# Optimization experiments

Measured on AMD Instinct MI355X. Metric: run time of the kernel, lower is better.

Reference implementation:

```python
import jax, jax.numpy as jnp
import numpy as np

N_NODES = 20000
DIM = 128
N_EDGES = 500000
BATCH = 16384
EPS = 1e-6  # torch.nn.PairwiseDistance default eps


def setup_inputs() -> dict:
    key = jax.random.key(0)
    k = jax.random.split(key, 8)
    edges = jax.random.randint(k[0], (2, N_EDGES), 0, N_NODES, dtype=jnp.int64 if jax.config.jax_enable_x64 else jnp.int32)
    nodes_p_star = jnp.sort(jax.random.randint(k[1], (BATCH,), 0, N_NODES))
    nodes_p = jnp.sort(jax.random.randint(k[2], (BATCH,), 0, N_NODES))
    # learned parameters, init in [-1, 1) as in the torch module
    beta_p = 2.0 * jax.random.uniform(k[3], (N_NODES,), dtype=jnp.float32) - 1.0
    beta_p_star = 2.0 * jax.random.uniform(k[4], (N_NODES,), dtype=jnp.float32) - 1.0
    p = 2.0 * jax.random.uniform(k[5], (N_NODES, DIM), dtype=jnp.float32) - 1.0
    p_star = 2.0 * jax.random.uniform(k[6], (N_NODES, DIM), dtype=jnp.float32) - 1.0
    return {
        "edges": edges,
        "nodes_p_star": nodes_p_star,
        "nodes_p": nodes_p,
        "beta_p": beta_p,
        "beta_p_star": beta_p_star,
        "p": p,
        "p_star": p_star,
    }


def reference(edges, nodes_p_star, nodes_p, beta_p, beta_p_star, p, p_star):
    # ---- link term: sum over observed edges of (beta - dist) ----
    beta_pair = beta_p_star[edges[0]] + beta_p[edges[1]]  # [E]
    diff = p[edges[0]] - p_star[edges[1]]                 # [E, D]
    # torch PairwiseDistance adds eps to the difference before the norm
    z_dist = jnp.sqrt(jnp.sum((diff + EPS) ** 2, axis=-1))
    link_term = jnp.sum(beta_pair - z_dist)

    # ---- non-link term: triu-masked sum of exp(beta - cdist) ----
    bps = beta_p_star[nodes_p_star]   # [Ns]
    bp = beta_p[nodes_p]              # [Np]
    ps = p_star[nodes_p_star]         # [Ns, D]
    pp = p[nodes_p]                   # [Np, D]
    beta_mat = bps[None, :] + bp[:, None]          # [Np, Ns]
    # cdist(ps, pp) -> [Ns, Np] via Gram trick
    sq = (jnp.sum(ps * ps, axis=-1)[:, None]
          + jnp.sum(pp * pp, axis=-1)[None, :]
          - 2.0 * jnp.einsum('nd,md->nm', ps, pp))
    dist_mat = jnp.sqrt(jnp.maximum(sq, 0.0))      # [Ns, Np]
    intensity = jnp.exp(beta_mat.T - dist_mat)     # [Ns, Np]
    non_link = jnp.sum(jnp.triu(intensity, k=1))

    return -(link_term - non_link)
```

## Files before the change

### kernel.cpp

```cpp
#include <hip/hip_runtime.h>
#include <hip/hip_bf16.h>

#define N_NODES 20000
#define DIM 128
#define N_EDGES 500000
#define BATCH 16384
#define EPS 1e-6f
#define L2E 1.4426950408889634f

typedef _Float16 half8 __attribute__((ext_vector_type(8)));
typedef _Float16 half4_t __attribute__((ext_vector_type(4)));
typedef float f32x4 __attribute__((ext_vector_type(4)));

__device__ __forceinline__ float fast_sqrtf(float x) {
#if __has_builtin(__builtin_amdgcn_sqrtf)
    return __builtin_amdgcn_sqrtf(x);
#else
    return sqrtf(x);
#endif
}
__device__ __forceinline__ float fast_exp2f(float x) {
#if __has_builtin(__builtin_amdgcn_exp2f)
    return __builtin_amdgcn_exp2f(x);
#else
    return exp2f(x);
#endif
}

#define NB_TILE 8256

#define OFF_PGEMM 0
#define OFF_PSH   33280
#define OFF_PPH   4227584
#define OFF_N2S   8421888
#define OFF_N2P   8487424
#define OFF_BPS   8552960
#define OFF_BP    8618496
#define OFF_P16   8684032
#define OFF_PS16  13804032
#define OFF_END   18924032

__global__ __launch_bounds__(256) void prep_kernel(
    const float* __restrict__ p, const float* __restrict__ p_star,
    const float* __restrict__ beta_p, const float* __restrict__ beta_ps,
    const int* __restrict__ nodes_ps, const int* __restrict__ nodes_p,
    _Float16* __restrict__ Ah, float* __restrict__ n2A, float* __restrict__ bA2,
    _Float16* __restrict__ Bh, float* __restrict__ n2B, float* __restrict__ bB2,
    _Float16* __restrict__ p16, _Float16* __restrict__ ps16)
{
    const int bx = blockIdx.x;
    const int g = threadIdx.x & 31;
    const int r8 = threadIdx.x >> 5;
    if (bx < 4096) {
        const bool isA = bx < 2048;
        int row = (isA ? bx : bx - 2048) * 8 + r8;
        int id = isA ? nodes_ps[row] : nodes_p[row];
        const float* src = isA ? p_star : p;
        float4 v = ((const float4*)(src + (size_t)id * DIM))[g];
        half4_t o;
        o[0] = (_Float16)v.x; o[1] = (_Float16)v.y; o[2] = (_Float16)v.z; o[3] = (_Float16)v.w;
        _Float16* dst = isA ? Ah : Bh;
        *(half4_t*)(dst + (size_t)row * DIM + g * 4) = o;
        float nrm = v.x * v.x + v.y * v.y + v.z * v.z + v.w * v.w;
        #pragma unroll
        for (int m = 16; m >= 1; m >>= 1) nrm += __shfl_xor(nrm, m, 32);
        if (g == 0) {
            if (isA) { n2A[row] = nrm; bA2[row] = L2E * beta_ps[id]; }
            else     { n2B[row] = nrm; bB2[row] = L2E * beta_p[id]; }
        }
    } else {
        const bool isP = bx < 6596;
        int row = (isP ? bx - 4096 : bx - 6596) * 8 + r8;
        const float* src = isP ? p : p_star;
        _Float16* dst = isP ? p16 : ps16;
        float4 v = ((const float4*)(src + (size_t)row * DIM))[g];
        half4_t o;
        o[0] = (_Float16)v.x; o[1] = (_Float16)v.y; o[2] = (_Float16)v.z; o[3] = (_Float16)v.w;
        *(half4_t*)(dst + (size_t)row * DIM + g * 4) = o;
    }
}

__global__ __launch_bounds__(512, 4) void main_kernel(
    const _Float16* __restrict__ Ag, const _Float16* __restrict__ Bg,
    const float* __restrict__ n2A, const float* __restrict__ n2B,
    const float* __restrict__ bA2, const float* __restrict__ bB2,
    const int* __restrict__ edges,
    const float* __restrict__ beta_p, const float* __restrict__ beta_ps,
    const _Float16* __restrict__ p16, const _Float16* __restrict__ ps16,
    const float* __restrict__ pf, const float* __restrict__ psf, int use16,
    float* __restrict__ pgemm)
{
    const int bx = blockIdx.x, by = blockIdx.y;
    int ti, tj;
    const int len = 128 - by;
    if (bx < len) { ti = by; tj = by + bx; }
    else          { ti = 127 - by; tj = 127 - (bx - len); }
    const int i0 = ti * 128, j0 = tj * 128;
    const int bid = by * 129 + bx;
    const bool diag = (ti == tj);

    __shared__ __align__(16) _Float16 As[128][136];
    __shared__ __align__(16) _Float16 Bs[128][136];
    __shared__ float smr[8];

    const int tid = threadIdx.x;
    const int lane = tid & 63;
    const int w = tid >> 6;
    const int wm = w & 3;
    const int wn = w >> 2;
    const int quad = lane >> 4;
    const int lr = lane & 15;

    float lsum = 0.f;
    half8 ea[2], eb[2];
    float ebeta[2] = {0.f, 0.f};
    bool ev[2];
    {
        #pragma unroll
        for (int t = 0; t < 2; ++t) {
            int e = bid * 64 + w * 8 + quad * 2 + t;
            ev[t] = (e < N_EDGES);
            if (ev[t]) {
                int e0 = edges[e];
                int e1 = edges[N_EDGES + e];
                if (use16) {
                    ea[t] = *(const half8*)(p16 + (size_t)e0 * DIM + lr * 8);
                    eb[t] = *(const half8*)(ps16 + (size_t)e1 * DIM + lr * 8);
                    if (lr == 0) ebeta[t] = beta_ps[e0] + beta_p[e1];
                } else {
                    const float* ar = pf + (size_t)e0 * DIM + lr * 8;
                    const float* br = psf + (size_t)e1 * DIM + lr * 8;
                    float s = 0.f;
                    #pragma unroll
                    for (int k = 0; k < 8; ++k) {
                        float d = ar[k] - br[k] + EPS;
                        s = fmaf(d, d, s);
                    }
                    #pragma unroll
                    for (int m = 8; m >= 1; m >>= 1) s += __shfl_xor(s, m, 16);
                    if (lr == 0) lsum -= (beta_ps[e0] + beta_p[e1]) - fast_sqrtf(s);
                }
            }
        }
    }

    const int ilo = i0 + wm * 32, jlo = j0 + wn * 64;
    float4 n2i[2], bi[2];
    #pragma unroll
    for (int mi = 0; mi < 2; ++mi) {
        n2i[mi] = *(const float4*)&n2A[ilo + mi * 16 + quad * 4];
        bi[mi]  = *(const float4*)&bA2[ilo + mi * 16 + quad * 4];
    }
    float n2j[4], bj[4];
    #pragma unroll
    for (int ni = 0; ni < 4; ++ni) {
        n2j[ni] = n2B[jlo + ni * 16 + lr];
        bj[ni]  = bB2[jlo + ni * 16 + lr];
    }

    #pragma unroll
    for (int c = tid; c < 2048; c += 512) {
        int row = c >> 4, col = (c & 15) * 8;
        *(uint4*)&As[row][col] = *(const uint4*)(Ag + (size_t)(i0 + row) * DIM + col);
        *(uint4*)&Bs[row][col] = *(const uint4*)(Bg + (size_t)(j0 + row) * DIM + col);
    }
    __syncthreads();

    int cls = 0;
    if (diag) cls = (wn == 0) ? (wm >= 2 ? 2 : 1) : (wm >= 2 ? 1 : 0);

    if (cls != 2) {
        f32x4 acc[2][4] = {};
        #pragma unroll
        for (int ks = 0; ks < 4; ++ks) {
            int koff = ks * 32 + quad * 8;
            half8 af[2], bf[4];
            #pragma unroll
            for (int u = 0; u < 2; ++u) af[u] = *(const half8*)&As[wm * 32 + u * 16 + lr][koff];
            #pragma unroll
            for (int v = 0; v < 4; ++v) bf[v] = *(const half8*)&Bs[wn * 64 + v * 16 + lr][koff];
            #pragma unroll
            for (int mi = 0; mi < 2; ++mi)
                #pragma unroll
                for (int ni = 0; ni < 4; ++ni)
                    acc[mi][ni] = __builtin_amdgcn_mfma_f32_16x16x32_f16(af[mi], bf[ni], acc[mi][ni], 0, 0, 0);
        }

        if (cls == 0) {
            #pragma unroll
            for (int mi = 0; mi < 2; ++mi)
                #pragma unroll
                for (int ni = 0; ni < 4; ++ni) {
                    f32x4 d = acc[mi][ni];
                    #pragma unroll
                    for (int r = 0; r < 4; ++r) {
                        float tt = ((const float*)&n2i[mi])[r] + n2j[ni];
                        float sq = fmaxf(fmaf(d[r], -2.f, tt), 0.f);
                        float arg = fmaf(fast_sqrtf(sq), -L2E, ((const float*)&bi[mi])[r] + bj[ni]);
                        lsum += fast_exp2f(arg);
                    }
                }
        } else {
            #pragma unroll
            for (int mi = 0; mi < 2; ++mi)
                #pragma unroll
                for (int ni = 0; ni < 4; ++ni) {
                    f32x4 d = acc[mi][ni];
                    #pragma unroll
                    for (int r = 0; r < 4; ++r) {
                        int ig = ilo + mi * 16 + quad * 4 + r;
                        int jg = jlo + ni * 16 + lr;
                        float tt = ((const float*)&n2i[mi])[r] + n2j[ni];
                        float sq = fmaxf(fmaf(d[r], -2.f, tt), 0.f);
                        float arg = fmaf(fast_sqrtf(sq), -L2E, ((const float*)&bi[mi])[r] + bj[ni]);
                        float ex = fast_exp2f(arg);
                        if (jg > ig) lsum += ex;
                    }
                }
        }
    }

    if (use16) {
        #pragma unroll
        for (int t = 0; t < 2; ++t) {
            if (ev[t]) {
                float s = 0.f;
                #pragma unroll
                for (int k = 0; k < 8; ++k) {
                    float d = (float)ea[t][k] - (float)eb[t][k] + EPS;
                    s = fmaf(d, d, s);
                }
                #pragma unroll
                for (int m = 8; m >= 1; m >>= 1) s += __shfl_xor(s, m, 16);
                if (lr == 0) lsum -= ebeta[t] - fast_sqrtf(s);
            }
        }
    }

    #pragma unroll
    for (int m = 32; m >= 1; m >>= 1) lsum += __shfl_xor(lsum, m, 64);
    if (lane == 0) smr[w] = lsum;
    __syncthreads();
    if (tid == 0) {
        float t = 0.f;
        #pragma unroll
        for (int i = 0; i < 8; ++i) t += smr[i];
        pgemm[bid] = t;
    }
}

__global__ __launch_bounds__(1024) void reduce_kernel(
    const float* __restrict__ pg, float* __restrict__ out)
{
    float s = 0.f;
    for (int k = threadIdx.x; k < NB_TILE; k += 1024) s += pg[k];
    #pragma unroll
    for (int m = 32; m >= 1; m >>= 1) s += __shfl_xor(s, m, 64);
    __shared__ float sm[16];
    if ((threadIdx.x & 63) == 0) sm[threadIdx.x >> 6] = s;
    __syncthreads();
    if (threadIdx.x == 0) {
        float t = 0.f;
        #pragma unroll
        for (int i = 0; i < 16; ++i) t += sm[i];
        out[0] = t;
    }
}

extern "C" void kernel_launch(void* const* d_in, const int* in_sizes, int n_in,
                              void* d_out, int out_size, void* d_ws, size_t ws_size,
                              hipStream_t stream) {
    const int* edges = (const int*)d_in[0];
    const int* nodes_p_star = (const int*)d_in[1];
    const int* nodes_p = (const int*)d_in[2];
    const float* beta_p = (const float*)d_in[3];
    const float* beta_p_star = (const float*)d_in[4];
    const float* p = (const float*)d_in[5];
    const float* p_star = (const float*)d_in[6];

    char* ws = (char*)d_ws;
    float* pgemm = (float*)(ws + OFF_PGEMM);
    _Float16* psh = (_Float16*)(ws + OFF_PSH);
    _Float16* pph = (_Float16*)(ws + OFF_PPH);
    float* n2s = (float*)(ws + OFF_N2S);
    float* n2p = (float*)(ws + OFF_N2P);
    float* bps2 = (float*)(ws + OFF_BPS);
    float* bp2 = (float*)(ws + OFF_BP);
    _Float16* p16 = (_Float16*)(ws + OFF_P16);
    _Float16* ps16 = (_Float16*)(ws + OFF_PS16);

    const int use16 = (ws_size >= (size_t)OFF_END) ? 1 : 0;

    prep_kernel<<<9096, 256, 0, stream>>>(
        p, p_star, beta_p, beta_p_star, nodes_p_star, nodes_p,
        psh, n2s, bps2, pph, n2p, bp2, p16, ps16);

    main_kernel<<<dim3(129, 64), 512, 0, stream>>>(
        psh, pph, n2s, n2p, bps2, bp2,
        edges, beta_p, beta_p_star, p16, ps16, p, p_star, use16,
        pgemm);

    reduce_kernel<<<1, 1024, 0, stream>>>(pgemm, (float*)d_out);
}
```

Measured before the change: 193.4 us.

## Drop reduce kernel via atomics, halve LDS with K-split, vectorize fp16 conversion

Removes the separate reduction launch: prep zeroes the output and each main-kernel block atomically adds its partial sum. The main kernel now stages A/B tiles in two K-halves of 64, halving shared memory per block, with an extra barrier in exchange. The fp16 table conversion blocks each convert 512 contiguous float4s and are skipped when use16 is off. Atomic float accumulation makes the summation order nondeterministic.

```diff
diff --git a/kernel.cpp b/kernel.cpp
--- a/kernel.cpp
+++ b/kernel.cpp
@@ -27,9 +27,6 @@
 #endif
 }
 
-#define NB_TILE 8256
-
-#define OFF_PGEMM 0
 #define OFF_PSH   33280
 #define OFF_PPH   4227584
 #define OFF_N2S   8421888
@@ -46,12 +43,14 @@
     const int* __restrict__ nodes_ps, const int* __restrict__ nodes_p,
     _Float16* __restrict__ Ah, float* __restrict__ n2A, float* __restrict__ bA2,
     _Float16* __restrict__ Bh, float* __restrict__ n2B, float* __restrict__ bB2,
-    _Float16* __restrict__ p16, _Float16* __restrict__ ps16)
+    _Float16* __restrict__ p16, _Float16* __restrict__ ps16, int use16,
+    float* __restrict__ out)
 {
     const int bx = blockIdx.x;
-    const int g = threadIdx.x & 31;
-    const int r8 = threadIdx.x >> 5;
+    if (bx == 0 && threadIdx.x == 0) out[0] = 0.f;
     if (bx < 4096) {
+        const int g = threadIdx.x & 31;
+        const int r8 = threadIdx.x >> 5;
         const bool isA = bx < 2048;
         int row = (isA ? bx : bx - 2048) * 8 + r8;
         int id = isA ? nodes_ps[row] : nodes_p[row];
@@ -68,15 +67,20 @@
             if (isA) { n2A[row] = nrm; bA2[row] = L2E * beta_ps[id]; }
             else     { n2B[row] = nrm; bB2[row] = L2E * beta_p[id]; }
         }
-    } else {
-        const bool isP = bx < 6596;
-        int row = (isP ? bx - 4096 : bx - 6596) * 8 + r8;
+    } else if (use16) {
+        int b = bx - 4096;
+        const bool isP = b < 1250;
         const float* src = isP ? p : p_star;
         _Float16* dst = isP ? p16 : ps16;
-        float4 v = ((const float4*)(src + (size_t)row * DIM))[g];
-        half4_t o;
-        o[0] = (_Float16)v.x; o[1] = (_Float16)v.y; o[2] = (_Float16)v.z; o[3] = (_Float16)v.w;
-        *(half4_t*)(dst + (size_t)row * DIM + g * 4) = o;
+        int base = (isP ? b : b - 1250) * 512 + threadIdx.x;
+        #pragma unroll
+        for (int u = 0; u < 2; ++u) {
+            int f4 = base + u * 256;
+            float4 v = ((const float4*)src)[f4];
+            half4_t o;
+            o[0] = (_Float16)v.x; o[1] = (_Float16)v.y; o[2] = (_Float16)v.z; o[3] = (_Float16)v.w;
+            ((half4_t*)dst)[f4] = o;
+        }
     }
 }
 
@@ -88,7 +92,7 @@
     const float* __restrict__ beta_p, const float* __restrict__ beta_ps,
     const _Float16* __restrict__ p16, const _Float16* __restrict__ ps16,
     const float* __restrict__ pf, const float* __restrict__ psf, int use16,
-    float* __restrict__ pgemm)
+    float* __restrict__ out)
 {
     const int bx = blockIdx.x, by = blockIdx.y;
     int ti, tj;
@@ -99,8 +103,8 @@
     const int bid = by * 129 + bx;
     const bool diag = (ti == tj);
 
-    __shared__ __align__(16) _Float16 As[128][136];
-    __shared__ __align__(16) _Float16 Bs[128][136];
+    __shared__ __align__(16) _Float16 As[128][72];
+    __shared__ __align__(16) _Float16 Bs[128][72];
     __shared__ float smr[8];
 
     const int tid = threadIdx.x;
@@ -115,31 +119,29 @@
     half8 ea[2], eb[2];
     float ebeta[2] = {0.f, 0.f};
     bool ev[2];
-    {
-        #pragma unroll
-        for (int t = 0; t < 2; ++t) {
-            int e = bid * 64 + w * 8 + quad * 2 + t;
-            ev[t] = (e < N_EDGES);
-            if (ev[t]) {
-                int e0 = edges[e];
-                int e1 = edges[N_EDGES + e];
-                if (use16) {
-                    ea[t] = *(const half8*)(p16 + (size_t)e0 * DIM + lr * 8);
-                    eb[t] = *(const half8*)(ps16 + (size_t)e1 * DIM + lr * 8);
-                    if (lr == 0) ebeta[t] = beta_ps[e0] + beta_p[e1];
-                } else {
-                    const float* ar = pf + (size_t)e0 * DIM + lr * 8;
-                    const float* br = psf + (size_t)e1 * DIM + lr * 8;
-                    float s = 0.f;
-                    #pragma unroll
-                    for (int k = 0; k < 8; ++k) {
-                        float d = ar[k] - br[k] + EPS;
-                        s = fmaf(d, d, s);
-                    }
-                    #pragma unroll
-                    for (int m = 8; m >= 1; m >>= 1) s += __shfl_xor(s, m, 16);
-                    if (lr == 0) lsum -= (beta_ps[e0] + beta_p[e1]) - fast_sqrtf(s);
-                }
+    #pragma unroll
+    for (int t = 0; t < 2; ++t) {
+        int e = bid * 64 + w * 8 + quad * 2 + t;
+        ev[t] = (e < N_EDGES);
+        if (ev[t]) {
+            int e0 = edges[e];
+            int e1 = edges[N_EDGES + e];
+            if (use16) {
+                ea[t] = *(const half8*)(p16 + (size_t)e0 * DIM + lr * 8);
+                eb[t] = *(const half8*)(ps16 + (size_t)e1 * DIM + lr * 8);
+                if (lr == 0) ebeta[t] = beta_ps[e0] + beta_p[e1];
+            } else {
+                const float* ar = pf + (size_t)e0 * DIM + lr * 8;
+                const float* br = psf + (size_t)e1 * DIM + lr * 8;
+                float s = 0.f;
+                #pragma unroll
+                for (int k = 0; k < 8; ++k) {
+                    float d = ar[k] - br[k] + EPS;
+                    s = fmaf(d, d, s);
+                }
+                #pragma unroll
+                for (int m = 8; m >= 1; m >>= 1) s += __shfl_xor(s, m, 16);
+                if (lr == 0) lsum -= (beta_ps[e0] + beta_p[e1]) - fast_sqrtf(s);
             }
         }
     }
@@ -158,34 +160,39 @@
         bj[ni]  = bB2[jlo + ni * 16 + lr];
     }
 
-    #pragma unroll
-    for (int c = tid; c < 2048; c += 512) {
-        int row = c >> 4, col = (c & 15) * 8;
-        *(uint4*)&As[row][col] = *(const uint4*)(Ag + (size_t)(i0 + row) * DIM + col);
-        *(uint4*)&Bs[row][col] = *(const uint4*)(Bg + (size_t)(j0 + row) * DIM + col);
-    }
-    __syncthreads();
-
     int cls = 0;
     if (diag) cls = (wn == 0) ? (wm >= 2 ? 2 : 1) : (wm >= 2 ? 1 : 0);
 
+    f32x4 acc[2][4] = {};
+    #pragma unroll
+    for (int kh = 0; kh < 2; ++kh) {
+        if (kh) __syncthreads();
+        #pragma unroll
+        for (int c = tid; c < 1024; c += 512) {
+            int row = c >> 3, col = (c & 7) * 8;
+            *(uint4*)&As[row][col] = *(const uint4*)(Ag + (size_t)(i0 + row) * DIM + kh * 64 + col);
+            *(uint4*)&Bs[row][col] = *(const uint4*)(Bg + (size_t)(j0 + row) * DIM + kh * 64 + col);
+        }
+        __syncthreads();
+        if (cls != 2) {
+            #pragma unroll
+            for (int ks = 0; ks < 2; ++ks) {
+                int koff = ks * 32 + quad * 8;
+                half8 af[2], bf[4];
+                #pragma unroll
+                for (int u = 0; u < 2; ++u) af[u] = *(const half8*)&As[wm * 32 + u * 16 + lr][koff];
+                #pragma unroll
+                for (int v = 0; v < 4; ++v) bf[v] = *(const half8*)&Bs[wn * 64 + v * 16 + lr][koff];
+                #pragma unroll
+                for (int mi = 0; mi < 2; ++mi)
+                    #pragma unroll
+                    for (int ni = 0; ni < 4; ++ni)
+                        acc[mi][ni] = __builtin_amdgcn_mfma_f32_16x16x32_f16(af[mi], bf[ni], acc[mi][ni], 0, 0, 0);
+            }
+        }
+    }
+
     if (cls != 2) {
-        f32x4 acc[2][4] = {};
-        #pragma unroll
-        for (int ks = 0; ks < 4; ++ks) {
-            int koff = ks * 32 + quad * 8;
-            half8 af[2], bf[4];
-            #pragma unroll
-            for (int u = 0; u < 2; ++u) af[u] = *(const half8*)&As[wm * 32 + u * 16 + lr][koff];
-            #pragma unroll
-            for (int v = 0; v < 4; ++v) bf[v] = *(const half8*)&Bs[wn * 64 + v * 16 + lr][koff];
-            #pragma unroll
-            for (int mi = 0; mi < 2; ++mi)
-                #pragma unroll
-                for (int ni = 0; ni < 4; ++ni)
-                    acc[mi][ni] = __builtin_amdgcn_mfma_f32_16x16x32_f16(af[mi], bf[ni], acc[mi][ni], 0, 0, 0);
-        }
-
         if (cls == 0) {
             #pragma unroll
             for (int mi = 0; mi < 2; ++mi)
@@ -245,25 +252,7 @@
         float t = 0.f;
         #pragma unroll
         for (int i = 0; i < 8; ++i) t += smr[i];
-        pgemm[bid] = t;
-    }
-}
-
-__global__ __launch_bounds__(1024) void reduce_kernel(
-    const float* __restrict__ pg, float* __restrict__ out)
-{
-    float s = 0.f;
-    for (int k = threadIdx.x; k < NB_TILE; k += 1024) s += pg[k];
-    #pragma unroll
-    for (int m = 32; m >= 1; m >>= 1) s += __shfl_xor(s, m, 64);
-    __shared__ float sm[16];
-    if ((threadIdx.x & 63) == 0) sm[threadIdx.x >> 6] = s;
-    __syncthreads();
-    if (threadIdx.x == 0) {
-        float t = 0.f;
-        #pragma unroll
-        for (int i = 0; i < 16; ++i) t += sm[i];
-        out[0] = t;
+        atomicAdd(out, t);
     }
 }
 
@@ -279,7 +268,6 @@
     const float* p_star = (const float*)d_in[6];
 
     char* ws = (char*)d_ws;
-    float* pgemm = (float*)(ws + OFF_PGEMM);
     _Float16* psh = (_Float16*)(ws + OFF_PSH);
     _Float16* pph = (_Float16*)(ws + OFF_PPH);
     float* n2s = (float*)(ws + OFF_N2S);
@@ -291,14 +279,12 @@
 
     const int use16 = (ws_size >= (size_t)OFF_END) ? 1 : 0;
 
-    prep_kernel<<<9096, 256, 0, stream>>>(
+    prep_kernel<<<6596, 256, 0, stream>>>(
         p, p_star, beta_p, beta_p_star, nodes_p_star, nodes_p,
-        psh, n2s, bps2, pph, n2p, bp2, p16, ps16);
+        psh, n2s, bps2, pph, n2p, bp2, p16, ps16, use16, (float*)d_out);
 
     main_kernel<<<dim3(129, 64), 512, 0, stream>>>(
         psh, pph, n2s, n2p, bps2, bp2,
         edges, beta_p, beta_p_star, p16, ps16, p, p_star, use16,
-        pgemm);
-
-    reduce_kernel<<<1, 1024, 0, stream>>>(pgemm, (float*)d_out);
-}
+        (float*)d_out);
+}
```

Result: slower. 226.8 us (+17.2%).
